# Kernel tuning notes

Measured on AMD Instinct MI355X. Metric: run time of the kernel, lower is better.

Reference implementation:

```python
import jax, jax.numpy as jnp
import numpy as np

N_ENTS = 50000
N_RELS2 = 460  # num_rels * 2
H_DIM = 128
T = 8
E = 200000
M = 400000
RRELU_SLOPE = (1.0 / 8.0 + 1.0 / 3.0) / 2.0  # F.rrelu eval mode
EPS = 1e-12


def l2norm(x):
    # F.normalize(x) along last dim
    return x / jnp.maximum(jnp.linalg.norm(x, axis=-1, keepdims=True), EPS)


def gru_cell(x, h, W_ih, W_hh, b_ih, b_hh):
    # torch.nn.GRUCell math
    gi = x @ W_ih.T + b_ih
    gh = h @ W_hh.T + b_hh
    i_r, i_z, i_n = jnp.split(gi, 3, axis=-1)
    h_r, h_z, h_n = jnp.split(gh, 3, axis=-1)
    r = jax.nn.sigmoid(i_r + h_r)
    z = jax.nn.sigmoid(i_z + h_z)
    n = jnp.tanh(i_n + r * h_n)
    return (1.0 - z) * n + z * h


def rrelu(x):
    return jnp.where(x >= 0, x, RRELU_SLOPE * x)


def setup_inputs() -> dict:
    key = jax.random.key(0)
    ks = jax.random.split(key, 12)
    src = jax.random.randint(ks[0], (T, E), 0, N_ENTS, dtype=jnp.int32)
    dst = jax.random.randint(ks[1], (T, E), 0, N_ENTS, dtype=jnp.int32)
    etype = jax.random.randint(ks[2], (T, E), 0, N_RELS2, dtype=jnp.int32)
    r_to_e_idx = jax.random.randint(ks[3], (T, M), 0, N_ENTS, dtype=jnp.int32)
    rel_seg = jax.random.randint(ks[4], (T, M), 0, N_RELS2, dtype=jnp.int32)
    s = 1.0 / np.sqrt(H_DIM)
    dynamic_emb = jax.random.normal(ks[5], (N_ENTS, H_DIM), jnp.float32)
    emb_rel = jax.random.normal(ks[6], (N_RELS2, H_DIM), jnp.float32) * s
    gru_W_ih = jax.random.uniform(ks[7], (3 * H_DIM, 2 * H_DIM), jnp.float32, -s, s)
    gru_W_hh = jax.random.uniform(ks[8], (3 * H_DIM, H_DIM), jnp.float32, -s, s)
    gru_b_ih = jnp.zeros((3 * H_DIM,), jnp.float32)
    gru_b_hh = jnp.zeros((3 * H_DIM,), jnp.float32)
    rgcn_W = jax.random.normal(ks[9], (2, H_DIM, H_DIM), jnp.float32) * s  # 2 hidden layers
    time_gate_weight = jax.random.normal(ks[10], (H_DIM, H_DIM), jnp.float32) * s
    time_gate_bias = jnp.zeros((H_DIM,), jnp.float32)
    return {
        "src": src, "dst": dst, "etype": etype,
        "r_to_e_idx": r_to_e_idx, "rel_seg": rel_seg,
        "dynamic_emb": dynamic_emb, "emb_rel": emb_rel,
        "gru_W_ih": gru_W_ih, "gru_W_hh": gru_W_hh,
        "gru_b_ih": gru_b_ih, "gru_b_hh": gru_b_hh,
        "rgcn_W": rgcn_W,
        "time_gate_weight": time_gate_weight, "time_gate_bias": time_gate_bias,
    }


def reference(src, dst, etype, r_to_e_idx, rel_seg, dynamic_emb, emb_rel,
              gru_W_ih, gru_W_hh, gru_b_ih, gru_b_hh, rgcn_W,
              time_gate_weight, time_gate_bias):
    h_init = l2norm(dynamic_emb)  # layer_norm=True path

    def step(carry, xs):
        h, h0 = carry
        src_t, dst_t, etype_t, rte_t, rseg_t = xs
        # --- relation evolution: mean of incident entity embeddings per relation ---
        temp_e = h[rte_t]  # [M, d]
        sums = jax.ops.segment_sum(temp_e, rseg_t, num_segments=N_RELS2)
        cnts = jax.ops.segment_sum(jnp.ones((M,), h.dtype), rseg_t, num_segments=N_RELS2)
        x_mean = jnp.where(cnts[:, None] > 0, sums / jnp.maximum(cnts[:, None], 1.0), 0.0)
        x_input = jnp.concatenate([emb_rel, x_mean], axis=1)  # [2R, 2d]
        h0 = l2norm(gru_cell(x_input, h0, gru_W_ih, gru_W_hh, gru_b_ih, gru_b_hh))
        # --- RGCN (UnionRGCNLayer x2): msg=(h[src]+r[etype])@W, sum agg, 1/indeg norm, rrelu ---
        deg = jax.ops.segment_sum(jnp.ones((E,), h.dtype), dst_t, num_segments=N_ENTS)
        norm = jnp.where(deg > 0, 1.0 / jnp.maximum(deg, 1.0), 0.0)  # [N]
        nh = h
        for l in range(2):
            msg = (nh[src_t] + h0[etype_t]) @ rgcn_W[l]  # [E, d]
            agg = jax.ops.segment_sum(msg, dst_t, num_segments=N_ENTS) * norm[:, None]
            nh = rrelu(agg)
        current_h = l2norm(nh)
        # --- time gate fusion ---
        tw = jax.nn.sigmoid(h @ time_gate_weight + time_gate_bias)
        h_new = tw * current_h + (1.0 - tw) * h
        return (h_new, h0), h_new

    (_, h0_final), history = jax.lax.scan(
        step, (h_init, emb_rel), (src, dst, etype, r_to_e_idx, rel_seg))
    return history, h0_final  # [T, N, d], [2R, d]
```

## Files before the change

kernel.cpp:

```cpp
#include <hip/hip_runtime.h>
#include <math.h>

#define NENT 50000
#define NR2 460
#define HD 128
#define TS 8
#define EPC 200000
#define MPC 400000
#define RSLOPE 0.22916666666666666f
#define RBLK 128
#define NTOT (TS * NENT)
#define NB8 ((NTOT + 255) / 256)
#define SCAN2_PER ((NB8 + 255) / 256)
#define RSP 8

typedef __attribute__((ext_vector_type(8))) short bfrag;
typedef __attribute__((ext_vector_type(4))) float facc;

__device__ __forceinline__ float sigm(float x) { return 1.0f / (1.0f + expf(-x)); }
__device__ __forceinline__ float rrelu_f(float x) { return x >= 0.0f ? x : RSLOPE * x; }
__device__ __forceinline__ unsigned short f2bf_rne(float x) {
  unsigned u = __float_as_uint(x);
  unsigned r = (u + 0x7FFFu + ((u >> 16) & 1u)) >> 16;
  return (unsigned short)r;
}
__device__ __forceinline__ float bf2f(unsigned short b) {
  return __uint_as_float(((unsigned)b) << 16);
}

__global__ __launch_bounds__(HD) void k_l2rows(const float* __restrict__ in,
                                               float* __restrict__ out) {
  int r = blockIdx.x, j = threadIdx.x;
  __shared__ float red[HD];
  float v = in[(size_t)r * HD + j];
  red[j] = v * v;
  __syncthreads();
  for (int s = HD / 2; s > 0; s >>= 1) { if (j < s) red[j] += red[j + s]; __syncthreads(); }
  float rn = 1.0f / fmaxf(sqrtf(red[0]), 1e-12f);
  out[(size_t)r * HD + j] = v * rn;
}

__global__ void k_hist(const int* __restrict__ idx, int* __restrict__ cnt,
                       int n, int per_t, int stride) {
  int i = blockIdx.x * blockDim.x + threadIdx.x;
  int gs = gridDim.x * blockDim.x;
  for (; i < n; i += gs) atomicAdd(&cnt[(i / per_t) * stride + idx[i]], 1);
}

__global__ __launch_bounds__(256) void k_histR2(const int* __restrict__ rseg,
                                                int* __restrict__ blkcnt) {
  __shared__ int h[NR2];
  int b = blockIdx.x, t = blockIdx.y, tid = threadIdx.x;
  for (int i = tid; i < NR2; i += 256) h[i] = 0;
  __syncthreads();
  const int* rs = rseg + (size_t)t * MPC;
  int chunk = (MPC + RBLK - 1) / RBLK;
  int m0 = b * chunk, m1 = min(MPC, m0 + chunk);
  for (int m = m0 + tid; m < m1; m += 256) atomicAdd(&h[rs[m]], 1);
  __syncthreads();
  for (int i = tid; i < NR2; i += 256) blkcnt[((size_t)(t * RBLK + b)) * NR2 + i] = h[i];
}

__global__ __launch_bounds__(256) void k_scanR2a(const int* __restrict__ blkcnt,
                                                 int* __restrict__ tot) {
  int idx = blockIdx.x * 256 + threadIdx.x;
  if (idx >= TS * NR2) return;
  int t = idx / NR2, r = idx - t * NR2;
  int s = 0;
  for (int b = 0; b < RBLK; ++b) s += blkcnt[((size_t)(t * RBLK + b)) * NR2 + r];
  tot[idx] = s;
}

__global__ __launch_bounds__(512) void k_scanR2b(const int* __restrict__ tot,
    int* __restrict__ offsR, float* __restrict__ invc) {
  __shared__ int s[TS * NR2];
  int tid = threadIdx.x;
  for (int i = tid; i < TS * NR2; i += 512) s[i] = tot[i];
  __syncthreads();
  if (tid < TS) {
    int acc = tid * MPC;
    for (int r = 0; r < NR2; ++r) { int c = s[tid * NR2 + r]; s[tid * NR2 + r] = acc; acc += c; }
  }
  __syncthreads();
  for (int i = tid; i < TS * NR2; i += 512) {
    offsR[i] = s[i];
    int c = tot[i];
    invc[i] = c > 0 ? 1.0f / (float)c : 0.0f;
  }
  if (tid == 0) offsR[TS * NR2] = TS * MPC;
}

__global__ __launch_bounds__(256) void k_scanR2c(int* __restrict__ blkcnt,
                                                 const int* __restrict__ offsR) {
  int gw = (blockIdx.x * blockDim.x + threadIdx.x) >> 6;
  int lane = threadIdx.x & 63;
  if (gw >= TS * NR2) return;
  int t = gw / NR2, r = gw - t * NR2;
  size_t i0 = ((size_t)(t * RBLK + lane * 2)) * NR2 + r;
  size_t i1 = ((size_t)(t * RBLK + lane * 2 + 1)) * NR2 + r;
  int v0 = blkcnt[i0], v1 = blkcnt[i1];
  int s = v0 + v1;
  int sc = s;
  #pragma unroll
  for (int o = 1; o < 64; o <<= 1) {
    int x = __shfl_up(sc, o, 64);
    if (lane >= o) sc += x;
  }
  int basev = offsR[gw] + (sc - s);
  blkcnt[i0] = basev;
  blkcnt[i1] = basev + v0;
}

__global__ __launch_bounds__(256) void k_scatterR2(const int* __restrict__ rte,
    const int* __restrict__ rseg, const int* __restrict__ blkbase,
    int* __restrict__ out) {
  __shared__ int cur[NR2];
  int b = blockIdx.x, t = blockIdx.y, tid = threadIdx.x;
  for (int i = tid; i < NR2; i += 256) cur[i] = blkbase[((size_t)(t * RBLK + b)) * NR2 + i];
  __syncthreads();
  const int* rs = rseg + (size_t)t * MPC;
  const int* re = rte + (size_t)t * MPC;
  int chunk = (MPC + RBLK - 1) / RBLK;
  int m0 = b * chunk, m1 = min(MPC, m0 + chunk);
  for (int m = m0 + tid; m < m1; m += 256) {
    int r = rs[m];
    int p = atomicAdd(&cur[r], 1);
    out[p] = re[m];
  }
}

__global__ __launch_bounds__(256) void k_scan1(const int* __restrict__ deg,
    int* __restrict__ offs, float* __restrict__ normv, int* __restrict__ bsum) {
  __shared__ int sd[256];
  int b = blockIdx.x, tid = threadIdx.x;
  int i = b * 256 + tid;
  int v = (i < NTOT) ? deg[i] : 0;
  sd[tid] = v;
  __syncthreads();
  for (int o = 1; o < 256; o <<= 1) {
    int x = (tid >= o) ? sd[tid - o] : 0;
    __syncthreads();
    sd[tid] += x;
    __syncthreads();
  }
  if (i < NTOT) {
    offs[i] = sd[tid] - v;
    normv[i] = v > 0 ? 1.0f / (float)v : 0.0f;
  }
  if (tid == 255) bsum[b] = sd[255];
}

__global__ __launch_bounds__(256) void k_scan2(int* __restrict__ bsum) {
  __shared__ int part[256];
  int tid = threadIdx.x;
  int base = tid * SCAN2_PER;
  int local[SCAN2_PER];
  int s = 0;
  #pragma unroll
  for (int k = 0; k < SCAN2_PER; ++k) {
    int v = (base + k < NB8) ? bsum[base + k] : 0;
    local[k] = s;
    s += v;
  }
  part[tid] = s;
  __syncthreads();
  for (int o = 1; o < 256; o <<= 1) {
    int x = (tid >= o) ? part[tid - o] : 0;
    __syncthreads();
    part[tid] += x;
    __syncthreads();
  }
  int pre = (tid > 0) ? part[tid - 1] : 0;
  #pragma unroll
  for (int k = 0; k < SCAN2_PER; ++k)
    if (base + k < NB8) bsum[base + k] = pre + local[k];
}

__global__ __launch_bounds__(256) void k_scan3(int* __restrict__ offs, int* __restrict__ cur,
                                               const int* __restrict__ bsum) {
  int b = blockIdx.x;
  int i = b * 256 + threadIdx.x;
  if (i < NTOT) {
    int o = offs[i] + bsum[b];
    offs[i] = o;
    cur[i] = o;
  }
  if (b == 0 && threadIdx.x == 0) offs[NTOT] = TS * EPC;
}

__global__ void k_scatterE(const int* __restrict__ src, const int* __restrict__ dst,
                           const int* __restrict__ ety, int* __restrict__ cur,
                           int2* __restrict__ se) {
  int i = blockIdx.x * blockDim.x + threadIdx.x;
  int gs = gridDim.x * blockDim.x;
  for (; i < TS * EPC; i += gs) {
    int t = i / EPC;
    int d = dst[i];
    int p = atomicAdd(&cur[t * NENT + d], 1);
    se[p] = make_int2(src[i], ety[i]);
  }
}

__global__ __launch_bounds__(256) void k_prepW(const float* __restrict__ W,
    unsigned short* __restrict__ hi, unsigned short* __restrict__ lo) {
  int t = blockIdx.x * 256 + threadIdx.x;
  int nt = t >> 8, ks = (t >> 6) & 3, lane = t & 63;
  int n = nt * 16 + (lane & 15);
  int k0 = ks * 32 + ((lane >> 4) << 3);
  #pragma unroll
  for (int j = 0; j < 8; ++j) {
    float v = W[(k0 + j) * HD + n];
    unsigned short h = f2bf_rne(v);
    hi[t * 8 + j] = h;
    lo[t * 8 + j] = f2bf_rne(v - bf2f(h));
  }
}

__global__ __launch_bounds__(256) void k_relmean(const float* __restrict__ h,
    const int* __restrict__ offs, const int* __restrict__ rte_csr,
    float* __restrict__ partials) {
  int rel = blockIdx.x, sp = blockIdx.y;
  int o0 = offs[rel], o1 = offs[rel + 1];
  int n = o1 - o0;
  int s0 = o0 + ((n * sp) >> 3);
  int s1 = o0 + ((n * (sp + 1)) >> 3);
  int w = threadIdx.x >> 6, lane = threadIdx.x & 63;
  const float2* h2 = (const float2*)h;
  float sx = 0.f, sy = 0.f;
  int p = s0 + w;
  for (; p + 4 < s1; p += 8) {
    int i0 = rte_csr[p];
    int i1 = rte_csr[p + 4];
    float2 v0 = h2[(size_t)i0 * 64 + lane];
    float2 v1 = h2[(size_t)i1 * 64 + lane];
    sx += v0.x + v1.x; sy += v0.y + v1.y;
  }
  for (; p < s1; p += 4) {
    int i0 = rte_csr[p];
    float2 v0 = h2[(size_t)i0 * 64 + lane];
    sx += v0.x; sy += v0.y;
  }
  __shared__ float red[4][HD];
  red[w][lane * 2] = sx;
  red[w][lane * 2 + 1] = sy;
  __syncthreads();
  if (threadIdx.x < HD) {
    int j = threadIdx.x;
    float t = red[0][j] + red[1][j] + red[2][j] + red[3][j];
    partials[((size_t)sp * NR2 + rel) * HD + j] = t;
  }
}

__global__ __launch_bounds__(HD) void k_gru(
    const float* __restrict__ partials, const float* __restrict__ invcnt,
    const float* __restrict__ emb_rel, const float* __restrict__ h0s,
    const float* __restrict__ Wih, const float* __restrict__ Whh,
    const float* __restrict__ bih, const float* __restrict__ bhh,
    float* __restrict__ h0d) {
  int r = blockIdx.x, j = threadIdx.x;
  __shared__ __align__(16) float xr[2 * HD];
  __shared__ __align__(16) float hh[HD];
  __shared__ float red[HD];
  float inv = invcnt[r];
  xr[j] = emb_rel[r * HD + j];
  float xm = 0.f;
  #pragma unroll
  for (int sp = 0; sp < RSP; ++sp) xm += partials[((size_t)sp * NR2 + r) * HD + j];
  xr[HD + j] = xm * inv;
  float hv0 = h0s[r * HD + j];
  hh[j] = hv0;
  __syncthreads();
  float gr = bih[j], gz = bih[HD + j], gn = bih[2 * HD + j];
  const float4* W4 = (const float4*)Wih;
  int rowA = j * 64, rowB = (j + HD) * 64, rowC = (j + 2 * HD) * 64;
  #pragma unroll 4
  for (int k4 = 0; k4 < 64; ++k4) {
    float4 xa = ((const float4*)xr)[k4];
    float4 w0 = W4[rowA + k4];
    float4 w1 = W4[rowB + k4];
    float4 w2 = W4[rowC + k4];
    gr += w0.x * xa.x + w0.y * xa.y + w0.z * xa.z + w0.w * xa.w;
    gz += w1.x * xa.x + w1.y * xa.y + w1.z * xa.z + w1.w * xa.w;
    gn += w2.x * xa.x + w2.y * xa.y + w2.z * xa.z + w2.w * xa.w;
  }
  float hr = bhh[j], hz = bhh[HD + j], hn = bhh[2 * HD + j];
  const float4* Wh4 = (const float4*)Whh;
  int rA = j * 32, rB = (j + HD) * 32, rC = (j + 2 * HD) * 32;
  #pragma unroll 4
  for (int k4 = 0; k4 < 32; ++k4) {
    float4 xa = ((const float4*)hh)[k4];
    float4 w0 = Wh4[rA + k4];
    float4 w1 = Wh4[rB + k4];
    float4 w2 = Wh4[rC + k4];
    hr += w0.x * xa.x + w0.y * xa.y + w0.z * xa.z + w0.w * xa.w;
    hz += w1.x * xa.x + w1.y * xa.y + w1.z * xa.z + w1.w * xa.w;
    hn += w2.x * xa.x + w2.y * xa.y + w2.z * xa.z + w2.w * xa.w;
  }
  float rg = sigm(gr + hr);
  float zg = sigm(gz + hz);
  float ng = tanhf(gn + rg * hn);
  float hv = (1.0f - zg) * ng + zg * hv0;
  red[j] = hv * hv;
  __syncthreads();
  for (int s = HD / 2; s > 0; s >>= 1) { if (j < s) red[j] += red[j + s]; __syncthreads(); }
  float rn = 1.0f / fmaxf(sqrtf(red[0]), 1e-12f);
  h0d[r * HD + j] = hv * rn;
}

__global__ __launch_bounds__(256) void k_edge_csr(
    const float* __restrict__ nh, const float* __restrict__ h0,
    const int* __restrict__ offs, const int2* __restrict__ se,
    const float* __restrict__ norm, float* __restrict__ agg) {
  int gw = (blockIdx.x * blockDim.x + threadIdx.x) >> 6;
  int lane = threadIdx.x & 63;
  if (gw >= NENT) return;
  int o0 = offs[gw], o1 = offs[gw + 1];
  const float2* nh2 = (const float2*)nh;
  const float2* h02 = (const float2*)h0;
  float sx = 0.f, sy = 0.f;
  int p = o0;
  for (; p + 2 <= o1; p += 2) {
    int2 a = se[p];
    int2 b = se[p + 1];
    float2 va = nh2[(size_t)a.x * 64 + lane];
    float2 ra = h02[(size_t)a.y * 64 + lane];
    float2 vb = nh2[(size_t)b.x * 64 + lane];
    float2 rb = h02[(size_t)b.y * 64 + lane];
    sx += (va.x + ra.x) + (vb.x + rb.x);
    sy += (va.y + ra.y) + (vb.y + rb.y);
  }
  if (p < o1) {
    int2 a = se[p];
    float2 va = nh2[(size_t)a.x * 64 + lane];
    float2 ra = h02[(size_t)a.y * 64 + lane];
    sx += va.x + ra.x;
    sy += va.y + ra.y;
  }
  float nm = norm[gw];
  ((float2*)agg)[(size_t)gw * 64 + lane] = make_float2(sx * nm, sy * nm);
}

__global__ __launch_bounds__(256) void k_mm_mfma(
    float* __restrict__ A, const unsigned short* __restrict__ wHi,
    const unsigned short* __restrict__ wLo, int nrows) {
  __shared__ __align__(16) unsigned short AsH[64 * 128];
  __shared__ __align__(16) unsigned short AsL[64 * 128];
  int tid = threadIdx.x;
  int base = blockIdx.x * 64;
  const float4* A4 = (const float4*)A;
  #pragma unroll
  for (int it = 0; it < 8; ++it) {
    int idx = tid + it * 256;
    int r = idx >> 5, c4 = idx & 31;
    int c0 = c4 * 4;
    float4 v = make_float4(0.f, 0.f, 0.f, 0.f);
    if (base + r < nrows) v = A4[(size_t)(base + r) * 32 + c4];
    int chunk = (c0 >> 3) ^ (r & 7);
    int p = r * 128 + chunk * 8 + (c0 & 7);
    unsigned short h0 = f2bf_rne(v.x), h1 = f2bf_rne(v.y);
    unsigned short h2 = f2bf_rne(v.z), h3 = f2bf_rne(v.w);
    ushort4 hv; hv.x = h0; hv.y = h1; hv.z = h2; hv.w = h3;
    *(ushort4*)&AsH[p] = hv;
    ushort4 lv;
    lv.x = f2bf_rne(v.x - bf2f(h0)); lv.y = f2bf_rne(v.y - bf2f(h1));
    lv.z = f2bf_rne(v.z - bf2f(h2)); lv.w = f2bf_rne(v.w - bf2f(h3));
    *(ushort4*)&AsL[p] = lv;
  }
  __syncthreads();
  int w = tid >> 6, lane = tid & 63;
  int lrow = lane & 15, lk = lane >> 4;
  facc acc[8];
  #pragma unroll
  for (int nt = 0; nt < 8; ++nt) acc[nt] = (facc){0.f, 0.f, 0.f, 0.f};
  int arow = w * 16 + lrow;
  #pragma unroll
  for (int ks = 0; ks < 4; ++ks) {
    int chunk = (ks * 4 + lk) ^ (arow & 7);
    int p = arow * 128 + chunk * 8;
    bfrag aH = *(const bfrag*)&AsH[p];
    bfrag aL = *(const bfrag*)&AsL[p];
    #pragma unroll
    for (int nt = 0; nt < 8; ++nt) {
      int fi = ((nt * 4 + ks) * 64 + lane) * 8;
      bfrag bH = *(const bfrag*)&wHi[fi];
      bfrag bL = *(const bfrag*)&wLo[fi];
      acc[nt] = __builtin_amdgcn_mfma_f32_16x16x32_bf16(aH, bH, acc[nt], 0, 0, 0);
      acc[nt] = __builtin_amdgcn_mfma_f32_16x16x32_bf16(aH, bL, acc[nt], 0, 0, 0);
      acc[nt] = __builtin_amdgcn_mfma_f32_16x16x32_bf16(aL, bH, acc[nt], 0, 0, 0);
    }
  }
  #pragma unroll
  for (int nt = 0; nt < 8; ++nt)
    #pragma unroll
    for (int r = 0; r < 4; ++r) {
      int row = base + w * 16 + lk * 4 + r;
      if (row < nrows) A[(size_t)row * HD + nt * 16 + lrow] = rrelu_f(acc[nt][r]);
    }
}

__global__ __launch_bounds__(256) void k_final_mfma(
    const float* __restrict__ C, const float* __restrict__ Hin, float* __restrict__ Hout,
    const unsigned short* __restrict__ wHi, const unsigned short* __restrict__ wLo,
    const float* __restrict__ bias, int nrows) {
  __shared__ __align__(16) unsigned short AsH[64 * 128];
  __shared__ __align__(16) unsigned short AsL[64 * 128];
  int tid = threadIdx.x;
  int base = blockIdx.x * 64;
  const float4* H4 = (const float4*)Hin;
  #pragma unroll
  for (int it = 0; it < 8; ++it) {
    int idx = tid + it * 256;
    int r = idx >> 5, c4 = idx & 31;
    int c0 = c4 * 4;
    float4 v = make_float4(0.f, 0.f, 0.f, 0.f);
    if (base + r < nrows) v = H4[(size_t)(base + r) * 32 + c4];
    int chunk = (c0 >> 3) ^ (r & 7);
    int p = r * 128 + chunk * 8 + (c0 & 7);
    unsigned short h0 = f2bf_rne(v.x), h1 = f2bf_rne(v.y);
    unsigned short h2 = f2bf_rne(v.z), h3 = f2bf_rne(v.w);
    ushort4 hv; hv.x = h0; hv.y = h1; hv.z = h2; hv.w = h3;
    *(ushort4*)&AsH[p] = hv;
    ushort4 lv;
    lv.x = f2bf_rne(v.x - bf2f(h0)); lv.y = f2bf_rne(v.y - bf2f(h1));
    lv.z = f2bf_rne(v.z - bf2f(h2)); lv.w = f2bf_rne(v.w - bf2f(h3));
    *(ushort4*)&AsL[p] = lv;
  }
  __syncthreads();
  int w = tid >> 6, lane = tid & 63;
  int lrow = lane & 15, lk = lane >> 4;
  facc acc[8];
  #pragma unroll
  for (int nt = 0; nt < 8; ++nt) acc[nt] = (facc){0.f, 0.f, 0.f, 0.f};
  int arow = w * 16 + lrow;
  #pragma unroll
  for (int ks = 0; ks < 4; ++ks) {
    int chunk = (ks * 4 + lk) ^ (arow & 7);
    int p = arow * 128 + chunk * 8;
    bfrag aH = *(const bfrag*)&AsH[p];
    bfrag aL = *(const bfrag*)&AsL[p];
    #pragma unroll
    for (int nt = 0; nt < 8; ++nt) {
      int fi = ((nt * 4 + ks) * 64 + lane) * 8;
      bfrag bH = *(const bfrag*)&wHi[fi];
      bfrag bL = *(const bfrag*)&wLo[fi];
      acc[nt] = __builtin_amdgcn_mfma_f32_16x16x32_bf16(aH, bH, acc[nt], 0, 0, 0);
      acc[nt] = __builtin_amdgcn_mfma_f32_16x16x32_bf16(aH, bL, acc[nt], 0, 0, 0);
      acc[nt] = __builtin_amdgcn_mfma_f32_16x16x32_bf16(aL, bH, acc[nt], 0, 0, 0);
    }
  }
  float cv[8][4];
  float ss[4] = {0.f, 0.f, 0.f, 0.f};
  #pragma unroll
  for (int r = 0; r < 4; ++r) {
    int row = base + w * 16 + lk * 4 + r;
    int rok = row < nrows;
    #pragma unroll
    for (int nt = 0; nt < 8; ++nt) {
      float x = rok ? C[(size_t)row * HD + nt * 16 + lrow] : 0.f;
      cv[nt][r] = x;
      ss[r] += x * x;
    }
  }
  #pragma unroll
  for (int r = 0; r < 4; ++r) {
    #pragma unroll
    for (int o = 1; o < 16; o <<= 1) ss[r] += __shfl_xor(ss[r], o, 64);
    ss[r] = 1.0f / fmaxf(sqrtf(ss[r]), 1e-12f);
  }
  #pragma unroll
  for (int r = 0; r < 4; ++r) {
    int row = base + w * 16 + lk * 4 + r;
    if (row >= nrows) continue;
    #pragma unroll
    for (int nt = 0; nt < 8; ++nt) {
      int col = nt * 16 + lrow;
      float hv = Hin[(size_t)row * HD + col];
      float tw = sigm(acc[nt][r] + bias[col]);
      Hout[(size_t)row * HD + col] = tw * (cv[nt][r] * ss[r]) + (1.0f - tw) * hv;
    }
  }
}

extern "C" void kernel_launch(void* const* d_in, const int* in_sizes, int n_in,
                              void* d_out, int out_size, void* d_ws, size_t ws_size,
                              hipStream_t stream) {
  const int* src    = (const int*)d_in[0];
  const int* dst    = (const int*)d_in[1];
  const int* etype  = (const int*)d_in[2];
  const int* rte    = (const int*)d_in[3];
  const int* rseg   = (const int*)d_in[4];
  const float* dyn  = (const float*)d_in[5];
  const float* emb_rel = (const float*)d_in[6];
  const float* W_ih = (const float*)d_in[7];
  const float* W_hh = (const float*)d_in[8];
  const float* b_ih = (const float*)d_in[9];
  const float* b_hh = (const float*)d_in[10];
  const float* rgcnW = (const float*)d_in[11];
  const float* tgW  = (const float*)d_in[12];
  const float* tgB  = (const float*)d_in[13];
  float* out = (float*)d_out;
  (void)in_sizes; (void)n_in; (void)out_size; (void)ws_size;

  float* ws = (float*)d_ws;
  size_t off = 0;
  float* agg1    = ws + off; off += (size_t)NENT * HD;
  float* agg2    = ws + off; off += (size_t)NENT * HD;
  float* parts   = ws + off; off += (size_t)RSP * NR2 * HD;
  float* h0a     = ws + off; off += (size_t)NR2 * HD;
  float* h0b     = ws + off; off += (size_t)NR2 * HD;
  float* normv8  = ws + off; off += NTOT;
  float* invc8   = ws + off; off += TS * NR2;
  off = (off + 3) & ~(size_t)3;
  unsigned short* wf = (unsigned short*)(ws + off);
  unsigned short* w1H = wf;            unsigned short* w1L = wf + 16384;
  unsigned short* w2H = wf + 32768;    unsigned short* w2L = wf + 49152;
  unsigned short* wtH = wf + 65536;    unsigned short* wtL = wf + 81920;
  off += (6 * 16384) / 2;
  off = (off + 1) & ~(size_t)1;
  int2* csr_se8  = (int2*)(ws + off); off += (size_t)2 * TS * EPC;
  int* csr_rte8  = (int*)(ws + off);  off += (size_t)TS * MPC;
  int* degE8     = (int*)(ws + off);  off += NTOT;
  int* offsE8    = (int*)(ws + off);  off += NTOT + 2;
  int* curE8     = (int*)(ws + off);  off += NTOT;
  int* bsum      = (int*)(ws + off);  off += NB8;
  int* blkcntR8  = (int*)(ws + off);  off += (size_t)TS * RBLK * NR2;
  int* offsR8    = (int*)(ws + off);  off += TS * NR2 + 2;
  int* totR      = (int*)(ws + off);  off += TS * NR2;

  hipMemsetAsync(degE8, 0, (size_t)NTOT * sizeof(int), stream);
  k_hist<<<2048, 256, 0, stream>>>(dst, degE8, TS * EPC, EPC, NENT);
  k_scan1<<<NB8, 256, 0, stream>>>(degE8, offsE8, normv8, bsum);
  k_scan2<<<1, 256, 0, stream>>>(bsum);
  k_scan3<<<NB8, 256, 0, stream>>>(offsE8, curE8, bsum);
  k_scatterE<<<2048, 256, 0, stream>>>(src, dst, etype, curE8, csr_se8);
  k_histR2<<<dim3(RBLK, TS), 256, 0, stream>>>(rseg, blkcntR8);
  k_scanR2a<<<(TS * NR2 + 255) / 256, 256, 0, stream>>>(blkcntR8, totR);
  k_scanR2b<<<1, 512, 0, stream>>>(totR, offsR8, invc8);
  k_scanR2c<<<(TS * NR2 * 64 + 255) / 256, 256, 0, stream>>>(blkcntR8, offsR8);
  k_scatterR2<<<dim3(RBLK, TS), 256, 0, stream>>>(rte, rseg, blkcntR8, csr_rte8);
  k_prepW<<<8, 256, 0, stream>>>(rgcnW, w1H, w1L);
  k_prepW<<<8, 256, 0, stream>>>(rgcnW + HD * HD, w2H, w2L);
  k_prepW<<<8, 256, 0, stream>>>(tgW, wtH, wtL);

  k_l2rows<<<NENT, HD, 0, stream>>>(dyn, out);

  float* h0bufs[2] = {h0a, h0b};
  for (int t = 0; t < TS; ++t) {
    const float* h = out + (size_t)(t == 0 ? 0 : (t - 1)) * NENT * HD;
    float* hout = out + (size_t)t * NENT * HD;
    const float* h0s = (t == 0) ? emb_rel : h0bufs[(t - 1) & 1];
    float* h0d = h0bufs[t & 1];

    k_relmean<<<dim3(NR2, RSP), 256, 0, stream>>>(h, offsR8 + t * NR2, csr_rte8, parts);
    k_gru<<<NR2, HD, 0, stream>>>(parts, invc8 + t * NR2, emb_rel, h0s,
                                  W_ih, W_hh, b_ih, b_hh, h0d);

    k_edge_csr<<<(NENT * 64 + 255) / 256, 256, 0, stream>>>(
        h, h0d, offsE8 + t * NENT, csr_se8, normv8 + t * NENT, agg1);
    k_mm_mfma<<<(NENT + 63) / 64, 256, 0, stream>>>(agg1, w1H, w1L, NENT);
    k_edge_csr<<<(NENT * 64 + 255) / 256, 256, 0, stream>>>(
        agg1, h0d, offsE8 + t * NENT, csr_se8, normv8 + t * NENT, agg2);
    k_mm_mfma<<<(NENT + 63) / 64, 256, 0, stream>>>(agg2, w2H, w2L, NENT);

    k_final_mfma<<<(NENT + 63) / 64, 256, 0, stream>>>(agg2, h, hout, wtH, wtL, tgB, NENT);
  }
  hipMemcpyAsync(out + (size_t)TS * NENT * HD, h0bufs[(TS - 1) & 1],
                 (size_t)NR2 * HD * sizeof(float), hipMemcpyDeviceToDevice, stream);
}
```

Baseline: 1.786 ms.

## Gather bf16 copies of node features and pack edge records into 32 bits

Producers of entity features (l2rows, the first RGCN matmul, the time-gate kernel) now also write a bf16 copy. The relation-mean and edge-aggregation gathers read that copy, halving the bytes fetched per random row access. Edge CSR entries pack src<<9|etype into one 32-bit word instead of an int2, halving index traffic. This trades accuracy in the gathered sums for bandwidth and adds extra bf16 store traffic in the producers.

```diff
diff --git a/kernel.cpp b/kernel.cpp
--- a/kernel.cpp
+++ b/kernel.cpp
@@ -27,9 +27,12 @@
 __device__ __forceinline__ float bf2f(unsigned short b) {
   return __uint_as_float(((unsigned)b) << 16);
 }
+__device__ __forceinline__ float bfLO(unsigned u) { return __uint_as_float(u << 16); }
+__device__ __forceinline__ float bfHI(unsigned u) { return __uint_as_float(u & 0xFFFF0000u); }
 
 __global__ __launch_bounds__(HD) void k_l2rows(const float* __restrict__ in,
-                                               float* __restrict__ out) {
+                                               float* __restrict__ out,
+                                               unsigned short* __restrict__ out_bf) {
   int r = blockIdx.x, j = threadIdx.x;
   __shared__ float red[HD];
   float v = in[(size_t)r * HD + j];
@@ -37,7 +40,9 @@
   __syncthreads();
   for (int s = HD / 2; s > 0; s >>= 1) { if (j < s) red[j] += red[j + s]; __syncthreads(); }
   float rn = 1.0f / fmaxf(sqrtf(red[0]), 1e-12f);
-  out[(size_t)r * HD + j] = v * rn;
+  float o = v * rn;
+  out[(size_t)r * HD + j] = o;
+  out_bf[(size_t)r * HD + j] = f2bf_rne(o);
 }
 
 __global__ void k_hist(const int* __restrict__ idx, int* __restrict__ cnt,
@@ -190,14 +195,14 @@
 
 __global__ void k_scatterE(const int* __restrict__ src, const int* __restrict__ dst,
                            const int* __restrict__ ety, int* __restrict__ cur,
-                           int2* __restrict__ se) {
+                           unsigned* __restrict__ se) {
   int i = blockIdx.x * blockDim.x + threadIdx.x;
   int gs = gridDim.x * blockDim.x;
   for (; i < TS * EPC; i += gs) {
     int t = i / EPC;
     int d = dst[i];
     int p = atomicAdd(&cur[t * NENT + d], 1);
-    se[p] = make_int2(src[i], ety[i]);
+    se[p] = ((unsigned)src[i] << 9) | (unsigned)ety[i];
   }
 }
 
@@ -216,7 +221,7 @@
   }
 }
 
-__global__ __launch_bounds__(256) void k_relmean(const float* __restrict__ h,
+__global__ __launch_bounds__(256) void k_relmean(const unsigned short* __restrict__ h_bf,
     const int* __restrict__ offs, const int* __restrict__ rte_csr,
     float* __restrict__ partials) {
   int rel = blockIdx.x, sp = blockIdx.y;
@@ -225,20 +230,22 @@
   int s0 = o0 + ((n * sp) >> 3);
   int s1 = o0 + ((n * (sp + 1)) >> 3);
   int w = threadIdx.x >> 6, lane = threadIdx.x & 63;
-  const float2* h2 = (const float2*)h;
+  const unsigned* h4 = (const unsigned*)h_bf;
   float sx = 0.f, sy = 0.f;
   int p = s0 + w;
   for (; p + 4 < s1; p += 8) {
     int i0 = rte_csr[p];
     int i1 = rte_csr[p + 4];
-    float2 v0 = h2[(size_t)i0 * 64 + lane];
-    float2 v1 = h2[(size_t)i1 * 64 + lane];
-    sx += v0.x + v1.x; sy += v0.y + v1.y;
+    unsigned u0 = h4[(size_t)i0 * 64 + lane];
+    unsigned u1 = h4[(size_t)i1 * 64 + lane];
+    sx += bfLO(u0) + bfLO(u1);
+    sy += bfHI(u0) + bfHI(u1);
   }
   for (; p < s1; p += 4) {
     int i0 = rte_csr[p];
-    float2 v0 = h2[(size_t)i0 * 64 + lane];
-    sx += v0.x; sy += v0.y;
+    unsigned u0 = h4[(size_t)i0 * 64 + lane];
+    sx += bfLO(u0);
+    sy += bfHI(u0);
   }
   __shared__ float red[4][HD];
   red[w][lane * 2] = sx;
@@ -308,41 +315,43 @@
 }
 
 __global__ __launch_bounds__(256) void k_edge_csr(
-    const float* __restrict__ nh, const float* __restrict__ h0,
-    const int* __restrict__ offs, const int2* __restrict__ se,
+    const unsigned short* __restrict__ nh_bf, const float* __restrict__ h0,
+    const int* __restrict__ offs, const unsigned* __restrict__ se,
     const float* __restrict__ norm, float* __restrict__ agg) {
   int gw = (blockIdx.x * blockDim.x + threadIdx.x) >> 6;
   int lane = threadIdx.x & 63;
   if (gw >= NENT) return;
   int o0 = offs[gw], o1 = offs[gw + 1];
-  const float2* nh2 = (const float2*)nh;
+  const unsigned* nh4 = (const unsigned*)nh_bf;
   const float2* h02 = (const float2*)h0;
   float sx = 0.f, sy = 0.f;
   int p = o0;
   for (; p + 2 <= o1; p += 2) {
-    int2 a = se[p];
-    int2 b = se[p + 1];
-    float2 va = nh2[(size_t)a.x * 64 + lane];
-    float2 ra = h02[(size_t)a.y * 64 + lane];
-    float2 vb = nh2[(size_t)b.x * 64 + lane];
-    float2 rb = h02[(size_t)b.y * 64 + lane];
-    sx += (va.x + ra.x) + (vb.x + rb.x);
-    sy += (va.y + ra.y) + (vb.y + rb.y);
+    unsigned e0 = se[p];
+    unsigned e1 = se[p + 1];
+    unsigned ua = nh4[(size_t)(e0 >> 9) * 64 + lane];
+    float2 ra = h02[(size_t)(e0 & 511u) * 64 + lane];
+    unsigned ub = nh4[(size_t)(e1 >> 9) * 64 + lane];
+    float2 rb = h02[(size_t)(e1 & 511u) * 64 + lane];
+    sx += (bfLO(ua) + ra.x) + (bfLO(ub) + rb.x);
+    sy += (bfHI(ua) + ra.y) + (bfHI(ub) + rb.y);
   }
   if (p < o1) {
-    int2 a = se[p];
-    float2 va = nh2[(size_t)a.x * 64 + lane];
-    float2 ra = h02[(size_t)a.y * 64 + lane];
-    sx += va.x + ra.x;
-    sy += va.y + ra.y;
+    unsigned e0 = se[p];
+    unsigned ua = nh4[(size_t)(e0 >> 9) * 64 + lane];
+    float2 ra = h02[(size_t)(e0 & 511u) * 64 + lane];
+    sx += bfLO(ua) + ra.x;
+    sy += bfHI(ua) + ra.y;
   }
   float nm = norm[gw];
   ((float2*)agg)[(size_t)gw * 64 + lane] = make_float2(sx * nm, sy * nm);
 }
 
+template<int OUT_BF>
 __global__ __launch_bounds__(256) void k_mm_mfma(
-    float* __restrict__ A, const unsigned short* __restrict__ wHi,
-    const unsigned short* __restrict__ wLo, int nrows) {
+    float* __restrict__ A, unsigned short* __restrict__ Abf,
+    const unsigned short* __restrict__ wHi, const unsigned short* __restrict__ wLo,
+    int nrows) {
   __shared__ __align__(16) unsigned short AsH[64 * 128];
   __shared__ __align__(16) unsigned short AsL[64 * 128];
   int tid = threadIdx.x;
@@ -394,12 +403,17 @@
     #pragma unroll
     for (int r = 0; r < 4; ++r) {
       int row = base + w * 16 + lk * 4 + r;
-      if (row < nrows) A[(size_t)row * HD + nt * 16 + lrow] = rrelu_f(acc[nt][r]);
+      if (row < nrows) {
+        float res = rrelu_f(acc[nt][r]);
+        if (OUT_BF) Abf[(size_t)row * HD + nt * 16 + lrow] = f2bf_rne(res);
+        else A[(size_t)row * HD + nt * 16 + lrow] = res;
+      }
     }
 }
 
 __global__ __launch_bounds__(256) void k_final_mfma(
     const float* __restrict__ C, const float* __restrict__ Hin, float* __restrict__ Hout,
+    unsigned short* __restrict__ Hout_bf,
     const unsigned short* __restrict__ wHi, const unsigned short* __restrict__ wLo,
     const float* __restrict__ bias, int nrows) {
   __shared__ __align__(16) unsigned short AsH[64 * 128];
@@ -476,7 +490,9 @@
       int col = nt * 16 + lrow;
       float hv = Hin[(size_t)row * HD + col];
       float tw = sigm(acc[nt][r] + bias[col]);
-      Hout[(size_t)row * HD + col] = tw * (cv[nt][r] * ss[r]) + (1.0f - tw) * hv;
+      float res = tw * (cv[nt][r] * ss[r]) + (1.0f - tw) * hv;
+      Hout[(size_t)row * HD + col] = res;
+      Hout_bf[(size_t)row * HD + col] = f2bf_rne(res);
     }
   }
 }
@@ -511,13 +527,14 @@
   float* normv8  = ws + off; off += NTOT;
   float* invc8   = ws + off; off += TS * NR2;
   off = (off + 3) & ~(size_t)3;
+  unsigned short* h_bf    = (unsigned short*)(ws + off); off += (size_t)NENT * HD / 2;
+  unsigned short* agg1_bf = (unsigned short*)(ws + off); off += (size_t)NENT * HD / 2;
   unsigned short* wf = (unsigned short*)(ws + off);
   unsigned short* w1H = wf;            unsigned short* w1L = wf + 16384;
   unsigned short* w2H = wf + 32768;    unsigned short* w2L = wf + 49152;
   unsigned short* wtH = wf + 65536;    unsigned short* wtL = wf + 81920;
   off += (6 * 16384) / 2;
-  off = (off + 1) & ~(size_t)1;
-  int2* csr_se8  = (int2*)(ws + off); off += (size_t)2 * TS * EPC;
+  unsigned* csr_se8 = (unsigned*)(ws + off); off += (size_t)TS * EPC;
   int* csr_rte8  = (int*)(ws + off);  off += (size_t)TS * MPC;
   int* degE8     = (int*)(ws + off);  off += NTOT;
   int* offsE8    = (int*)(ws + off);  off += NTOT + 2;
@@ -542,7 +559,7 @@
   k_prepW<<<8, 256, 0, stream>>>(rgcnW + HD * HD, w2H, w2L);
   k_prepW<<<8, 256, 0, stream>>>(tgW, wtH, wtL);
 
-  k_l2rows<<<NENT, HD, 0, stream>>>(dyn, out);
+  k_l2rows<<<NENT, HD, 0, stream>>>(dyn, out, h_bf);
 
   float* h0bufs[2] = {h0a, h0b};
   for (int t = 0; t < TS; ++t) {
@@ -551,18 +568,19 @@
     const float* h0s = (t == 0) ? emb_rel : h0bufs[(t - 1) & 1];
     float* h0d = h0bufs[t & 1];
 
-    k_relmean<<<dim3(NR2, RSP), 256, 0, stream>>>(h, offsR8 + t * NR2, csr_rte8, parts);
+    k_relmean<<<dim3(NR2, RSP), 256, 0, stream>>>(h_bf, offsR8 + t * NR2, csr_rte8, parts);
     k_gru<<<NR2, HD, 0, stream>>>(parts, invc8 + t * NR2, emb_rel, h0s,
                                   W_ih, W_hh, b_ih, b_hh, h0d);
 
     k_edge_csr<<<(NENT * 64 + 255) / 256, 256, 0, stream>>>(
-        h, h0d, offsE8 + t * NENT, csr_se8, normv8 + t * NENT, agg1);
-    k_mm_mfma<<<(NENT + 63) / 64, 256, 0, stream>>>(agg1, w1H, w1L, NENT);
+        h_bf, h0d, offsE8 + t * NENT, csr_se8, normv8 + t * NENT, agg1);
+    k_mm_mfma<1><<<(NENT + 63) / 64, 256, 0, stream>>>(agg1, agg1_bf, w1H, w1L, NENT);
     k_edge_csr<<<(NENT * 64 + 255) / 256, 256, 0, stream>>>(
-        agg1, h0d, offsE8 + t * NENT, csr_se8, normv8 + t * NENT, agg2);
-    k_mm_mfma<<<(NENT + 63) / 64, 256, 0, stream>>>(agg2, w2H, w2L, NENT);
-
-    k_final_mfma<<<(NENT + 63) / 64, 256, 0, stream>>>(agg2, h, hout, wtH, wtL, tgB, NENT);
+        agg1_bf, h0d, offsE8 + t * NENT, csr_se8, normv8 + t * NENT, agg2);
+    k_mm_mfma<0><<<(NENT + 63) / 64, 256, 0, stream>>>(agg2, (unsigned short*)nullptr,
+                                                       w2H, w2L, NENT);
+    k_final_mfma<<<(NENT + 63) / 64, 256, 0, stream>>>(agg2, h, hout, h_bf,
+                                                       wtH, wtL, tgB, NENT);
   }
   hipMemcpyAsync(out + (size_t)TS * NENT * HD, h0bufs[(TS - 1) & 1],
                  (size_t)NR2 * HD * sizeof(float), hipMemcpyDeviceToDevice, stream);
```

Measured after the change: 1.690 ms. -5.4%, faster.
